# Performance work log

Hardware: AMD Instinct MI355X
Metric: run time of the kernel (lower is better)

## Reference

```python
import jax, jax.numpy as jnp
import numpy as np

NUM_HEAD = 16


def setup_inputs() -> dict:
    key = jax.random.key(0)
    k1, k2, k3 = jax.random.split(key, 3)
    E = 1024
    x = jax.random.normal(k1, (4, 2048, E), dtype=jnp.float32)
    W1 = jax.random.normal(k2, (E, 3 * E), dtype=jnp.float32) * 0.02
    b1 = jnp.zeros((3 * E,), dtype=jnp.float32)
    W2 = jax.random.normal(k3, (E, E), dtype=jnp.float32) * 0.02
    b2 = jnp.zeros((E,), dtype=jnp.float32)
    return {"x": x, "W1": W1, "b1": b1, "W2": W2, "b2": b2}


def reference(x, W1, b1, W2, b2):
    # Fused QKV projection: (n, s, 3E)
    h = x @ W1 + b1
    n, s, _ = h.shape
    # Split into heads FIRST (matches torch reshape), then transpose: (n, H, s, 3*d_head)
    h = h.reshape(n, s, NUM_HEAD, -1).transpose(0, 2, 1, 3)
    # Chunk last dim into q, k, v: each (n, H, s, d_head)
    q, k, v = jnp.split(h, 3, axis=-1)
    dk = jnp.asarray(v.shape[-1], x.dtype) ** 0.5
    # Naive full S x S attention (faithful to source)
    w = jnp.einsum("nhqd,nhkd->nhqk", q, k) / dk
    w = jax.nn.softmax(w, axis=-1)  # dropout1 is identity at eval
    att = jnp.einsum("nhqk,nhkd->nhqd", w, v)
    att = att.transpose(0, 2, 1, 3).reshape(n, s, -1)  # (n, s, E)
    return att @ W2 + b2  # dropout2 identity at eval
```

## Files before the change

### kernel.cpp

```cpp
#include <hip/hip_runtime.h>
#include <math.h>
#include <stdint.h>
#include <stddef.h>


#define SEQ    2048
#define NB     4
#define E_DIM  1024
#define N1     3072
#define M_TOK  8192
#define NHEAD  16
#define DHEAD  64

typedef __attribute__((ext_vector_type(4))) float    floatx4;
typedef __attribute__((ext_vector_type(8))) short    shortx8;
typedef __attribute__((ext_vector_type(4))) short    shortx4;
typedef __attribute__((ext_vector_type(4))) unsigned short ushortx4;

#if __has_builtin(__builtin_amdgcn_exp2f)
#define EXP2(x) __builtin_amdgcn_exp2f(x)
#else
#define EXP2(x) __expf((x) * 0.6931471805599453f)
#endif

#define MFMA_K16(a, b, c) \
    __builtin_amdgcn_mfma_f32_16x16x16bf16_1k((a), (b), (c), 0, 0, 0)

__device__ __forceinline__ unsigned short f2bf(float f) {
    union { float f; unsigned u; } v; v.f = f;
    unsigned r = (v.u + 0x7FFFu + ((v.u >> 16) & 1u)) >> 16;
    return (unsigned short)r;
}
__device__ __forceinline__ unsigned fbits(float f) {
    union { float f; unsigned u; } v; v.f = f; return v.u;
}

__device__ __forceinline__ void gl_lds16(const void* g, void* l) {
    __builtin_amdgcn_global_load_lds(
        (const __attribute__((address_space(1))) unsigned int*)g,
        (__attribute__((address_space(3))) unsigned int*)l, 16, 0, 0);
}

__global__ __launch_bounds__(256) void cvt_bf16(
    const float* __restrict__ in, unsigned short* __restrict__ out)
{
    const size_t i = ((size_t)blockIdx.x * 256 + threadIdx.x) * 8;
    float4 a = *(const float4*)(in + i);
    float4 b = *(const float4*)(in + i + 4);
    ushortx4 o0 = { f2bf(a.x), f2bf(a.y), f2bf(a.z), f2bf(a.w) };
    ushortx4 o1 = { f2bf(b.x), f2bf(b.y), f2bf(b.z), f2bf(b.w) };
    *(ushortx4*)(out + i)     = o0;
    *(ushortx4*)(out + i + 4) = o1;
}

__global__ __launch_bounds__(256) void cvt_transpose(
    const float* __restrict__ W, unsigned short* __restrict__ Wt, int K, int N)
{
    __shared__ unsigned short tile[32][33];
    const int tx = threadIdx.x, ty = threadIdx.y;
    const int n0 = blockIdx.x * 32, k0 = blockIdx.y * 32;
#pragma unroll
    for (int r = 0; r < 4; ++r) {
        const int k = ty + r * 8;
        tile[tx][k] = f2bf(W[(size_t)(k0 + k) * N + n0 + tx]);
    }
    __syncthreads();
#pragma unroll
    for (int r = 0; r < 4; ++r) {
        const int n = ty + r * 8;
        Wt[(size_t)(n0 + n) * K + k0 + tx] = tile[n][tx];
    }
}

template <bool OUT_BF16, bool FUSE>
__global__ __launch_bounds__(256) void gemm_bf16(
    const short* __restrict__ A, const short* __restrict__ Bt,
    const float* __restrict__ bias, void* __restrict__ Cout,
    unsigned short* __restrict__ Vt,
    int M, int N, int K)
{
    __shared__ short As[128 * 32];
    __shared__ short Bs[128 * 32];

    const int t    = threadIdx.x;
    const int lane = t & 63, w = t >> 6;
    const int quad = lane >> 4, l15 = lane & 15;
    const int bm = blockIdx.y * 128, bn = blockIdx.x * 128;
    const int m0w = (w >> 1) * 64, n0w = (w & 1) * 64;

    const int lrow = lane >> 2;
    const int lcol = (lane & 3) * 8;
    const short* Ag0 = A  + (size_t)(bm + (2 * w + 0) * 16 + lrow) * K + lcol;
    const short* Ag1 = A  + (size_t)(bm + (2 * w + 1) * 16 + lrow) * K + lcol;
    const short* Bg0 = Bt + (size_t)(bn + (2 * w + 0) * 16 + lrow) * K + lcol;
    const short* Bg1 = Bt + (size_t)(bn + (2 * w + 1) * 16 + lrow) * K + lcol;
    short* Al0 = As + (2 * w + 0) * 512;
    short* Al1 = As + (2 * w + 1) * 512;
    short* Bl0 = Bs + (2 * w + 0) * 512;
    short* Bl1 = Bs + (2 * w + 1) * 512;

    floatx4 acc[4][4];
#pragma unroll
    for (int i = 0; i < 4; ++i)
#pragma unroll
        for (int j = 0; j < 4; ++j) acc[i][j] = (floatx4)0.f;

    for (int k0 = 0; k0 < K; k0 += 32) {
        __syncthreads();
        gl_lds16(Ag0, Al0); gl_lds16(Ag1, Al1);
        gl_lds16(Bg0, Bl0); gl_lds16(Bg1, Bl1);
        Ag0 += 32; Ag1 += 32; Bg0 += 32; Bg1 += 32;
        __syncthreads();

        shortx8 af[4], bf[4];
#pragma unroll
        for (int mi = 0; mi < 4; ++mi)
            af[mi] = *(const shortx8*)(As + (m0w + mi * 16 + l15) * 32 + quad * 8);
#pragma unroll
        for (int ni = 0; ni < 4; ++ni)
            bf[ni] = *(const shortx8*)(Bs + (n0w + ni * 16 + l15) * 32 + quad * 8);
#pragma unroll
        for (int mi = 0; mi < 4; ++mi)
#pragma unroll
            for (int ni = 0; ni < 4; ++ni)
                acc[mi][ni] = __builtin_amdgcn_mfma_f32_16x16x32_bf16(
                    af[mi], bf[ni], acc[mi][ni], 0, 0, 0);
    }

    float bv[4];
#pragma unroll
    for (int ni = 0; ni < 4; ++ni) bv[ni] = bias[bn + n0w + ni * 16 + l15];

#pragma unroll
    for (int ni = 0; ni < 4; ++ni) {
        const int col   = bn + n0w + ni * 16 + l15;
        const int cm    = col % 192;
        const int vhead = col / 192;
#pragma unroll
        for (int mi = 0; mi < 4; ++mi) {
            const int row0 = bm + m0w + mi * 16 + quad * 4;
            float v[4];
#pragma unroll
            for (int r = 0; r < 4; ++r) v[r] = acc[mi][ni][r] + bv[ni];
            if (OUT_BF16) {
                if (FUSE && cm < DHEAD) {
#pragma unroll
                    for (int r = 0; r < 4; ++r) v[r] *= 0.18033688011112042f;
                }
                unsigned short* H = (unsigned short*)Cout;
#pragma unroll
                for (int r = 0; r < 4; ++r)
                    H[(size_t)(row0 + r) * N + col] = f2bf(v[r]);
                if (FUSE && cm >= 2 * DHEAD) {
                    const int nb = row0 >> 11;
                    const int s  = row0 & 2047;
                    const int d  = cm - 2 * DHEAD;
                    ushortx4 pk = { f2bf(v[0]), f2bf(v[1]), f2bf(v[2]), f2bf(v[3]) };
                    *(ushortx4*)(Vt + ((size_t)(nb * NHEAD + vhead) * DHEAD + d) * SEQ + s) = pk;
                }
            } else {
                float* C = (float*)Cout;
#pragma unroll
                for (int r = 0; r < 4; ++r)
                    C[(size_t)(row0 + r) * N + col] = v[r];
            }
        }
    }
}

__global__ __launch_bounds__(256, 4) void attn_mfma(
    const short* __restrict__ h, const short* __restrict__ Vt,
    unsigned short* __restrict__ att)
{
    __shared__ short Ks[2][64 * 64];
    __shared__ short Vs[2][64 * 64];

    const int t    = threadIdx.x;
    const int lane = t & 63, w = t >> 6;
    const int quad = lane >> 4, l15 = lane & 15;
    const int r7   = l15 & 7;
    const int bh = blockIdx.x, n = bh >> 4, head = bh & 15;
    const int q0 = blockIdx.y * 128 + w * 32;

    const short* hQ  = h + (size_t)n * SEQ * N1 + head * (3 * DHEAD);
    const short* hK  = hQ + DHEAD;
    const short* Vtb = Vt + (size_t)bh * DHEAD * SEQ;

    const int srow = t >> 2;
    const int sc0  = (t & 3) * 2;
    const int sk   = srow & 7;
    const short* gK = hK  + (size_t)srow * N1  + sc0 * 8;
    const short* gV = Vtb + (size_t)srow * SEQ + sc0 * 8;
    const int oL0 = srow * 64 + ((sc0    ) ^ sk) * 8;
    const int oL1 = srow * 64 + ((sc0 + 1) ^ sk) * 8;

    shortx8 qf[2][2];
#pragma unroll
    for (int qt = 0; qt < 2; ++qt)
#pragma unroll
        for (int kt = 0; kt < 2; ++kt)
            qf[qt][kt] = *(const shortx8*)(hQ + (size_t)(q0 + qt * 16 + l15) * N1
                                           + kt * 32 + quad * 8);

    floatx4 O[2][4];
    floatx4 Osum[2];
#pragma unroll
    for (int qt = 0; qt < 2; ++qt) {
        Osum[qt] = (floatx4)0.f;
#pragma unroll
        for (int dt = 0; dt < 4; ++dt) O[qt][dt] = (floatx4)0.f;
    }

    const shortx4 ones = { (short)0x3F80, (short)0x3F80, (short)0x3F80, (short)0x3F80 };

    const int NT = SEQ / 64;

    int4 ka = *(const int4*)gK, kb = *(const int4*)(gK + 8);
    int4 va = *(const int4*)gV, vb = *(const int4*)(gV + 8);
    *(int4*)(&Ks[0][oL0]) = ka; *(int4*)(&Ks[0][oL1]) = kb;
    *(int4*)(&Vs[0][oL0]) = va; *(int4*)(&Vs[0][oL1]) = vb;
    gK += (size_t)64 * N1; gV += 64;

    for (int it = 0; it < NT; ++it) {
        const int buf = it & 1;
        __syncthreads();

        const bool more = (it + 1 < NT);
        if (more) {
            ka = *(const int4*)gK; kb = *(const int4*)(gK + 8);
            va = *(const int4*)gV; vb = *(const int4*)(gV + 8);
            gK += (size_t)64 * N1; gV += 64;
        }

        const short* Kb = &Ks[buf][0];
        const short* Vb = &Vs[buf][0];

#pragma unroll
        for (int sl = 0; sl < 4; ++sl) {
            const short* krow = Kb + (sl * 16 + l15) * 64;
            shortx8 kf0 = *(const shortx8*)(krow + ((quad ^ r7) * 8));
            shortx8 kf1 = *(const shortx8*)(krow + (((quad ^ 4) ^ r7) * 8));
            shortx4 vf[4];
#pragma unroll
            for (int dt = 0; dt < 4; ++dt)
                vf[dt] = *(const shortx4*)(Vb + (dt * 16 + l15) * 64
                                           + (((sl * 4 + quad) ^ (r7 << 1)) << 2));

            shortx4 pa[2];
#pragma unroll
            for (int qt = 0; qt < 2; ++qt) {
                floatx4 s = __builtin_amdgcn_mfma_f32_16x16x32_bf16(
                    kf0, qf[qt][0], (floatx4)0.f, 0, 0, 0);
                s = __builtin_amdgcn_mfma_f32_16x16x32_bf16(
                    kf1, qf[qt][1], s, 0, 0, 0);
                const float p0 = EXP2(s[0]);
                const float p1 = EXP2(s[1]);
                const float p2 = EXP2(s[2]);
                const float p3 = EXP2(s[3]);
                union { uint2 u; shortx4 v; } cv;
                cv.u.x = __builtin_amdgcn_perm(fbits(p1), fbits(p0), 0x07060302u);
                cv.u.y = __builtin_amdgcn_perm(fbits(p3), fbits(p2), 0x07060302u);
                pa[qt] = cv.v;
            }

#pragma unroll
            for (int qt = 0; qt < 2; ++qt) {
                Osum[qt] = MFMA_K16(pa[qt], ones, Osum[qt]);
#pragma unroll
                for (int dt = 0; dt < 4; ++dt)
                    O[qt][dt] = MFMA_K16(pa[qt], vf[dt], O[qt][dt]);
            }
        }

        if (more) {
            short* Kn = &Ks[buf ^ 1][0];
            short* Vn = &Vs[buf ^ 1][0];
            *(int4*)(Kn + oL0) = ka; *(int4*)(Kn + oL1) = kb;
            *(int4*)(Vn + oL0) = va; *(int4*)(Vn + oL1) = vb;
        }
    }

    const size_t obase = ((size_t)n * SEQ + q0) * E_DIM + head * DHEAD;
#pragma unroll
    for (int qt = 0; qt < 2; ++qt)
#pragma unroll
        for (int r = 0; r < 4; ++r) {
            const float inv = 1.f / Osum[qt][r];
            const size_t row = obase + (size_t)(qt * 16 + quad * 4 + r) * E_DIM;
#pragma unroll
            for (int dt = 0; dt < 4; ++dt)
                att[row + dt * 16 + l15] = f2bf(O[qt][dt][r] * inv);
        }
}

extern "C" void kernel_launch(void* const* d_in, const int* in_sizes, int n_in,
                              void* d_out, int out_size, void* d_ws, size_t ws_size,
                              hipStream_t stream)
{
    const float* x  = (const float*)d_in[0];
    const float* W1 = (const float*)d_in[1];
    const float* b1 = (const float*)d_in[2];
    const float* W2 = (const float*)d_in[3];
    const float* b2 = (const float*)d_in[4];
    float* out = (float*)d_out;

    char* ws = (char*)d_ws;
    unsigned short* x_bf  = (unsigned short*)(ws);
    unsigned short* W1t   = (unsigned short*)(ws + (16u << 20));
    unsigned short* W2t   = (unsigned short*)(ws + (22u << 20));
    unsigned short* h_bf  = (unsigned short*)(ws + (24u << 20));
    unsigned short* attb  = (unsigned short*)(ws + (72u << 20));
    unsigned short* Vtw   = (unsigned short*)(ws + (88u << 20));

    cvt_bf16<<<dim3((M_TOK * E_DIM) / (256 * 8)), 256, 0, stream>>>(x, x_bf);
    cvt_transpose<<<dim3(N1 / 32, E_DIM / 32), dim3(32, 8), 0, stream>>>(W1, W1t, E_DIM, N1);
    cvt_transpose<<<dim3(E_DIM / 32, E_DIM / 32), dim3(32, 8), 0, stream>>>(W2, W2t, E_DIM, E_DIM);

    gemm_bf16<true, true><<<dim3(N1 / 128, M_TOK / 128), 256, 0, stream>>>(
        (const short*)x_bf, (const short*)W1t, b1, h_bf, Vtw, M_TOK, N1, E_DIM);

    attn_mfma<<<dim3(NB * NHEAD, SEQ / 128), 256, 0, stream>>>(
        (const short*)h_bf, (const short*)Vtw, attb);

    gemm_bf16<false, false><<<dim3(E_DIM / 128, M_TOK / 128), 256, 0, stream>>>(
        (const short*)attb, (const short*)W2t, b2, out, nullptr, M_TOK, E_DIM, E_DIM);
}
```

Baseline: 283.8 us.

## Double-buffer GEMM LDS tiles with K=64 stages and XOR swizzle

Rewrites the bf16 GEMM main loop to use two LDS buffers with 64-wide K tiles. Loads for stage k+2 are issued while stage k is computed, and explicit vmcnt waits replace the double __syncthreads per iteration. An XOR swizzle on the 16-byte chunk index is meant to avoid LDS bank conflicts on the fragment reads. This raises LDS use to 64 KB per block, which may reduce occupancy.

```diff
diff --git a/kernel.cpp b/kernel.cpp
--- a/kernel.cpp
+++ b/kernel.cpp
@@ -34,6 +34,9 @@
 __device__ __forceinline__ unsigned fbits(float f) {
     union { float f; unsigned u; } v; v.f = f; return v.u;
 }
+__device__ __forceinline__ float bitsf(unsigned u) {
+    union { unsigned u; float f; } v; v.u = u; return v.f;
+}
 
 __device__ __forceinline__ void gl_lds16(const void* g, void* l) {
     __builtin_amdgcn_global_load_lds(
@@ -79,8 +82,8 @@
     unsigned short* __restrict__ Vt,
     int M, int N, int K)
 {
-    __shared__ short As[128 * 32];
-    __shared__ short Bs[128 * 32];
+    __shared__ short As[2][128 * 64];
+    __shared__ short Bs[2][128 * 64];
 
     const int t    = threadIdx.x;
     const int lane = t & 63, w = t >> 6;
@@ -88,16 +91,12 @@
     const int bm = blockIdx.y * 128, bn = blockIdx.x * 128;
     const int m0w = (w >> 1) * 64, n0w = (w & 1) * 64;
 
-    const int lrow = lane >> 2;
-    const int lcol = (lane & 3) * 8;
-    const short* Ag0 = A  + (size_t)(bm + (2 * w + 0) * 16 + lrow) * K + lcol;
-    const short* Ag1 = A  + (size_t)(bm + (2 * w + 1) * 16 + lrow) * K + lcol;
-    const short* Bg0 = Bt + (size_t)(bn + (2 * w + 0) * 16 + lrow) * K + lcol;
-    const short* Bg1 = Bt + (size_t)(bn + (2 * w + 1) * 16 + lrow) * K + lcol;
-    short* Al0 = As + (2 * w + 0) * 512;
-    short* Al1 = As + (2 * w + 1) * 512;
-    short* Bl0 = Bs + (2 * w + 0) * 512;
-    short* Bl1 = Bs + (2 * w + 1) * 512;
+    const int srow   = t >> 3;
+    const int schunk = t & 7;
+    const int gch    = schunk ^ (srow & 7);
+    const short* Ag = A  + (size_t)(bm + srow) * K + gch * 8;
+    const short* Bg = Bt + (size_t)(bn + srow) * K + gch * 8;
+    const int sOff = srow * 64 + schunk * 8;
 
     floatx4 acc[4][4];
 #pragma unroll
@@ -105,27 +104,53 @@
 #pragma unroll
         for (int j = 0; j < 4; ++j) acc[i][j] = (floatx4)0.f;
 
-    for (int k0 = 0; k0 < K; k0 += 32) {
-        __syncthreads();
-        gl_lds16(Ag0, Al0); gl_lds16(Ag1, Al1);
-        gl_lds16(Bg0, Bl0); gl_lds16(Bg1, Bl1);
-        Ag0 += 32; Ag1 += 32; Bg0 += 32; Bg1 += 32;
-        __syncthreads();
-
-        shortx8 af[4], bf[4];
-#pragma unroll
-        for (int mi = 0; mi < 4; ++mi)
-            af[mi] = *(const shortx8*)(As + (m0w + mi * 16 + l15) * 32 + quad * 8);
-#pragma unroll
-        for (int ni = 0; ni < 4; ++ni)
-            bf[ni] = *(const shortx8*)(Bs + (n0w + ni * 16 + l15) * 32 + quad * 8);
-#pragma unroll
-        for (int mi = 0; mi < 4; ++mi)
+    const int NK = K >> 6;
+
+#define GEMM_STAGE(bufi, k0)                                                   \
+    {                                                                          \
+        _Pragma("unroll")                                                      \
+        for (int r = 0; r < 4; ++r) {                                          \
+            gl_lds16(Ag + (size_t)(r * 32) * K + (k0), &As[bufi][sOff + r * 32 * 64]); \
+            gl_lds16(Bg + (size_t)(r * 32) * K + (k0), &Bs[bufi][sOff + r * 32 * 64]); \
+        }                                                                      \
+    }
+
+    GEMM_STAGE(0, 0);
+    GEMM_STAGE(1, 64);
+
+    for (int kt = 0; kt < NK; ++kt) {
+        const int buf = kt & 1;
+        if (kt + 1 < NK) asm volatile("s_waitcnt vmcnt(8)" ::: "memory");
+        else             asm volatile("s_waitcnt vmcnt(0)" ::: "memory");
+        __builtin_amdgcn_sched_barrier(0);
+        __builtin_amdgcn_s_barrier();
+        __builtin_amdgcn_sched_barrier(0);
+
+#pragma unroll
+        for (int kk = 0; kk < 2; ++kk) {
+            shortx8 af[4], bf[4];
+#pragma unroll
+            for (int mi = 0; mi < 4; ++mi)
+                af[mi] = *(const shortx8*)(&As[buf][(m0w + mi * 16 + l15) * 64
+                                           + (((kk * 4 + quad) ^ (l15 & 7)) * 8)]);
 #pragma unroll
             for (int ni = 0; ni < 4; ++ni)
-                acc[mi][ni] = __builtin_amdgcn_mfma_f32_16x16x32_bf16(
-                    af[mi], bf[ni], acc[mi][ni], 0, 0, 0);
-    }
+                bf[ni] = *(const shortx8*)(&Bs[buf][(n0w + ni * 16 + l15) * 64
+                                           + (((kk * 4 + quad) ^ (l15 & 7)) * 8)]);
+#pragma unroll
+            for (int mi = 0; mi < 4; ++mi)
+#pragma unroll
+                for (int ni = 0; ni < 4; ++ni)
+                    acc[mi][ni] = __builtin_amdgcn_mfma_f32_16x16x32_bf16(
+                        af[mi], bf[ni], acc[mi][ni], 0, 0, 0);
+        }
+
+        __builtin_amdgcn_sched_barrier(0);
+        __builtin_amdgcn_s_barrier();
+        __builtin_amdgcn_sched_barrier(0);
+        if (kt + 2 < NK) GEMM_STAGE(buf, (kt + 2) * 64);
+    }
+#undef GEMM_STAGE
 
     float bv[4];
 #pragma unroll
```

After: 266.2 us. -6.2%, faster.
